# Kernel optimization log

Measured on AMD Instinct MI355X. Metric: run time of the kernel, lower is better.

## Reference

```python
import jax, jax.numpy as jnp
import numpy as np

EPS = 1e-6

def setup_inputs() -> dict:
    key = jax.random.key(0)
    kq, kk, kv = jax.random.split(key, 3)
    B, N, D = 4, 4096, 1024
    Q = jax.random.normal(kq, (B, N, D), dtype=jnp.float32)
    K = jax.random.normal(kk, (B, N, D), dtype=jnp.float32)
    V = jax.random.normal(kv, (B, N, D), dtype=jnp.float32)
    return {"Q": Q, "K": K, "V": V}

def reference(Q, K, V):
    # phi(x) = elu(x) + 1
    phi = lambda x: jax.nn.elu(x) + 1.0
    Q_phi = phi(Q)                                   # [B,N,D]
    K_phi = phi(K)                                   # [B,N,D]
    K_sum = K_phi.sum(axis=1)                        # [B,D]
    Z = jnp.einsum('bnd,bd->bn', Q_phi, K_sum) + EPS # [B,N]
    KV = jnp.einsum('bnd,bne->bde', K_phi, V)        # [B,D,E]
    context = jnp.einsum('bnd,bde->bne', Q_phi, KV)  # [B,N,E]
    out = context / Z[..., None]
    return out  # dropout is identity at inference (rate set to 0)
```

## Files before the change

kernel.cpp:

```cpp
#include <hip/hip_runtime.h>

#define BATCH 4
#define SEQ   4096
#define DIM   1024
#define EPS_F 1e-6f
#define KSPLIT 4

typedef __bf16 bf16_t;
typedef bf16_t bf16x8 __attribute__((ext_vector_type(8)));
typedef float  f32x4  __attribute__((ext_vector_type(4)));
typedef unsigned short u16x8 __attribute__((ext_vector_type(8)));

__device__ __forceinline__ unsigned short f2bf(float f) {
  unsigned u = __float_as_uint(f);
  u += 0x7FFFu + ((u >> 16) & 1u);
  return (unsigned short)(u >> 16);
}
__device__ __forceinline__ float bf2f(unsigned short h) {
  return __uint_as_float(((unsigned)h) << 16);
}
__device__ __forceinline__ float phi_f(float x) {
  return x > 0.f ? x + 1.f : __expf(x);
}

__global__ __launch_bounds__(256) void zero_f32(float* __restrict__ p, int n) {
  const int i = blockIdx.x * 256 + threadIdx.x;
  if (i < n) p[i] = 0.f;
}

template<bool PHI, bool KSUM>
__global__ __launch_bounds__(256) void phi_transpose(const float* __restrict__ in,
    unsigned short* __restrict__ out, float* __restrict__ ksum, int rows, int cols) {
  __shared__ float t[32][33];
  __shared__ float ps[8][32];
  const int bx = blockIdx.x * 32;
  const int by = blockIdx.y * 32;
  const size_t bo = (size_t)blockIdx.z * rows * cols;
  const int x = threadIdx.x, y = threadIdx.y;
  #pragma unroll
  for (int j = 0; j < 32; j += 8) {
    float v = in[bo + (size_t)(by + y + j) * cols + bx + x];
    if (PHI) v = phi_f(v);
    t[y + j][x] = v;
  }
  __syncthreads();
  #pragma unroll
  for (int j = 0; j < 32; j += 8)
    out[bo + (size_t)(bx + y + j) * rows + by + x] = f2bf(t[x][y + j]);
  if (KSUM) {
    float s = t[y][x] + t[y + 8][x] + t[y + 16][x] + t[y + 24][x];
    ps[y][x] = s;
    __syncthreads();
    if (y == 0) {
      float tot = 0.f;
      #pragma unroll
      for (int j = 0; j < 8; ++j) tot += ps[j][x];
      atomicAdd(&ksum[(size_t)blockIdx.z * cols + bx + x], tot);
    }
  }
}

__global__ __launch_bounds__(256) void phi_cast_qz(const float* __restrict__ Q,
    const float* __restrict__ Ksum, unsigned short* __restrict__ Qp,
    float* __restrict__ invZ) {
  const int row  = blockIdx.x * 4 + (threadIdx.x >> 6);
  const int lane = threadIdx.x & 63;
  const int b = row >> 12;
  const float* q  = Q + (size_t)row * DIM;
  const float* ks = Ksum + (size_t)b * DIM;
  float s = 0.f;
  #pragma unroll
  for (int c = 0; c < 2; ++c) {
    const int d0 = c * 512 + lane * 8;
    float4 v0 = *(const float4*)(q + d0);
    float4 v1 = *(const float4*)(q + d0 + 4);
    float4 k0 = *(const float4*)(ks + d0);
    float4 k1 = *(const float4*)(ks + d0 + 4);
    u16x8 o;
    o[0] = f2bf(phi_f(v0.x)); s += bf2f(o[0]) * k0.x;
    o[1] = f2bf(phi_f(v0.y)); s += bf2f(o[1]) * k0.y;
    o[2] = f2bf(phi_f(v0.z)); s += bf2f(o[2]) * k0.z;
    o[3] = f2bf(phi_f(v0.w)); s += bf2f(o[3]) * k0.w;
    o[4] = f2bf(phi_f(v1.x)); s += bf2f(o[4]) * k1.x;
    o[5] = f2bf(phi_f(v1.y)); s += bf2f(o[5]) * k1.y;
    o[6] = f2bf(phi_f(v1.z)); s += bf2f(o[6]) * k1.z;
    o[7] = f2bf(phi_f(v1.w)); s += bf2f(o[7]) * k1.w;
    *(u16x8*)(Qp + (size_t)row * DIM + d0) = o;
  }
  #pragma unroll
  for (int off = 32; off > 0; off >>= 1) s += __shfl_down(s, off);
  if (lane == 0) invZ[row] = 1.0f / (s + EPS_F);
}

__global__ __launch_bounds__(256) void reduce_kv(const unsigned short* __restrict__ P,
    unsigned short* __restrict__ KVt) {
  const size_t per = (size_t)DIM * DIM;
  const size_t i = ((size_t)blockIdx.x * 256 + threadIdx.x) * 8;
  const size_t b = blockIdx.y;
  const unsigned short* p = P + b * KSPLIT * per + i;
  float s[8] = {};
  #pragma unroll
  for (int sp = 0; sp < KSPLIT; ++sp) {
    u16x8 v = *(const u16x8*)(p + sp * per);
    #pragma unroll
    for (int j = 0; j < 8; ++j) s[j] += bf2f(v[j]);
  }
  u16x8 o;
  #pragma unroll
  for (int j = 0; j < 8; ++j) o[j] = f2bf(s[j]);
  *(u16x8*)(KVt + b * per + i) = o;
}

#define GLD(gp, lp) __builtin_amdgcn_global_load_lds( \
    (const __attribute__((address_space(1))) unsigned int*)(gp), \
    (__attribute__((address_space(3))) unsigned int*)(lp), 16, 0, 0)
#define BARRIER __builtin_amdgcn_s_barrier()
#define WAITV(n) asm volatile("s_waitcnt vmcnt(" #n ")" ::: "memory")

template<int EPI, int KS>
__global__ __launch_bounds__(512, 2) void gemm256_bt(
    const unsigned short* __restrict__ A, const unsigned short* __restrict__ Bm,
    void* __restrict__ Cv, const float* __restrict__ invZ,
    int M, int Nc, int K, int gx, int gy) {
  extern __shared__ unsigned short lds[];
  unsigned short* const As0 = lds;
  unsigned short* const As1 = lds + 16384;
  unsigned short* const Bs0 = lds + 32768;
  unsigned short* const Bs1 = lds + 49152;

  const int t    = threadIdx.x;
  const int wid  = t >> 6;
  const int lane = t & 63;
  const int id   = blockIdx.x;
  const int sw   = (id & 7) * (gridDim.x >> 3) + (id >> 3);
  const int bxi  = sw % gx;
  const int rem  = sw / gx;
  const int byi  = rem % gy;
  const int bz   = rem / gy;
  const int brow = byi * 256, bcol = bxi * 256;
  const size_t batch = bz / KS;
  const int split = bz % KS;
  const int Kc = K / KS;
  const unsigned short* Ab = A + batch * ((size_t)M * K) + (size_t)brow * K + (size_t)split * Kc;
  const unsigned short* Bb = Bm + batch * ((size_t)Nc * K) + (size_t)bcol * K + (size_t)split * Kc;

  const int srow_t = t >> 3;
  const int c_src  = (t & 7) ^ (srow_t & 7);
  const unsigned short* gA = Ab + (size_t)srow_t * K + c_src * 8;
  const unsigned short* gB = Bb + (size_t)((srow_t >> 5) * 64 + (srow_t & 31)) * K + c_src * 8;
  const int ldsAu = wid * 512;
  const int ldsBu = wid * 512 + (wid >> 2) * 2048;

  auto stageA = [&](unsigned short* D, int h, int kt) {
    GLD(gA + (size_t)(h * 64) * K + (size_t)kt * 64,       D + (h * 64) * 64 + ldsAu);
    GLD(gA + (size_t)(128 + h * 64) * K + (size_t)kt * 64, D + (128 + h * 64) * 64 + ldsAu);
  };
  auto stageB = [&](unsigned short* D, int h, int kt) {
    GLD(gB + (size_t)(h * 32) * K + (size_t)kt * 64,       D + (h * 32) * 64 + ldsBu);
    GLD(gB + (size_t)(128 + h * 32) * K + (size_t)kt * 64, D + (128 + h * 32) * 64 + ldsBu);
  };

  const int fr  = lane & 15;
  const int g   = lane >> 4;
  const int wrw = (wid >> 2) * 128;
  const int wcw = (wid & 3) * 64;
  const int ck0 = ((g)     ^ (fr & 7)) * 8;
  const int ck1 = ((4 + g) ^ (fr & 7)) * 8;

  f32x4 acc[8][4] = {};
  bf16x8 af[4][2], bf0[2][2], bf1[2][2];

#define LOADA(S, mh) { _Pragma("unroll") for (int m_ = 0; m_ < 4; ++m_) { \
    const int ro_ = (wrw + ((mh) * 4 + m_) * 16 + fr) * 64; \
    af[m_][0] = *(const bf16x8*)((S) + ro_ + ck0); \
    af[m_][1] = *(const bf16x8*)((S) + ro_ + ck1); } }
#define LOADB(S, nh, BF) { _Pragma("unroll") for (int n_ = 0; n_ < 2; ++n_) { \
    const int ro_ = (wcw + (nh) * 32 + n_ * 16 + fr) * 64; \
    BF[n_][0] = *(const bf16x8*)((S) + ro_ + ck0); \
    BF[n_][1] = *(const bf16x8*)((S) + ro_ + ck1); } }
#define QUAD(mh, nh, BF) { __builtin_amdgcn_s_setprio(1); \
    _Pragma("unroll") for (int m_ = 0; m_ < 4; ++m_) \
    _Pragma("unroll") for (int n_ = 0; n_ < 2; ++n_) \
    _Pragma("unroll") for (int k_ = 0; k_ < 2; ++k_) \
      acc[(mh) * 4 + m_][(nh) * 2 + n_] = __builtin_amdgcn_mfma_f32_16x16x32_bf16( \
          af[m_][k_], BF[n_][k_], acc[(mh) * 4 + m_][(nh) * 2 + n_], 0, 0, 0); \
    __builtin_amdgcn_s_setprio(0); }

  stageA(As0, 0, 0); stageB(Bs0, 0, 0); stageB(Bs0, 1, 0); stageA(As0, 1, 0);
  stageA(As1, 0, 1); stageB(Bs1, 0, 1); stageB(Bs1, 1, 1);
  WAITV(6);
  BARRIER;

  const int NITER = Kc >> 7;
  for (int i = 0; i < NITER - 1; ++i) {
    const int k2 = 2 * i;
    LOADA(As0, 0); LOADB(Bs0, 0, bf0); stageA(As1, 1, k2 + 1);
    BARRIER; QUAD(0, 0, bf0); BARRIER;
    LOADB(Bs0, 1, bf1); stageA(As0, 0, k2 + 2);
    BARRIER; QUAD(0, 1, bf1); BARRIER;
    LOADA(As0, 1); stageB(Bs0, 0, k2 + 2);
    BARRIER; QUAD(1, 0, bf0); BARRIER;
    stageB(Bs0, 1, k2 + 2); WAITV(6);
    BARRIER; QUAD(1, 1, bf1); BARRIER;
    LOADA(As1, 0); LOADB(Bs1, 0, bf0); stageA(As0, 1, k2 + 2);
    BARRIER; QUAD(0, 0, bf0); BARRIER;
    LOADB(Bs1, 1, bf1); stageA(As1, 0, k2 + 3);
    BARRIER; QUAD(0, 1, bf1); BARRIER;
    LOADA(As1, 1); stageB(Bs1, 0, k2 + 3);
    BARRIER; QUAD(1, 0, bf0); BARRIER;
    stageB(Bs1, 1, k2 + 3); WAITV(6);
    BARRIER; QUAD(1, 1, bf1); BARRIER;
  }
  {
    const int k2 = 2 * (NITER - 1);
    LOADA(As0, 0); LOADB(Bs0, 0, bf0); stageA(As1, 1, k2 + 1);
    BARRIER; QUAD(0, 0, bf0); BARRIER;
    LOADB(Bs0, 1, bf1);
    BARRIER; QUAD(0, 1, bf1); BARRIER;
    LOADA(As0, 1);
    BARRIER; QUAD(1, 0, bf0); BARRIER;
    WAITV(0);
    BARRIER; QUAD(1, 1, bf1); BARRIER;
    LOADA(As1, 0); LOADB(Bs1, 0, bf0);
    BARRIER; QUAD(0, 0, bf0); BARRIER;
    LOADB(Bs1, 1, bf1);
    BARRIER; QUAD(0, 1, bf1); BARRIER;
    LOADA(As1, 1);
    BARRIER; QUAD(1, 0, bf0); BARRIER;
    QUAD(1, 1, bf1);
  }
#undef LOADA
#undef LOADB
#undef QUAD

  if (EPI == 0) {
    unsigned short* Cb = (unsigned short*)Cv + (size_t)bz * M * Nc;
    #pragma unroll
    for (int m = 0; m < 8; ++m) {
      const int row = brow + wrw + m * 16 + g * 4;
      #pragma unroll
      for (int r = 0; r < 4; ++r)
        #pragma unroll
        for (int n = 0; n < 4; ++n)
          Cb[(size_t)(row + r) * Nc + bcol + wcw + n * 16 + fr] = f2bf(acc[m][n][r]);
    }
  } else {
    float* Cb = (float*)Cv + batch * ((size_t)M * Nc);
    const float* zb = invZ + batch * (size_t)M;
    #pragma unroll
    for (int m = 0; m < 8; ++m) {
      const int row = brow + wrw + m * 16 + g * 4;
      #pragma unroll
      for (int r = 0; r < 4; ++r) {
        const float z = zb[row + r];
        #pragma unroll
        for (int n = 0; n < 4; ++n)
          Cb[(size_t)(row + r) * Nc + bcol + wcw + n * 16 + fr] = acc[m][n][r] * z;
      }
    }
  }
}

extern "C" void kernel_launch(void* const* d_in, const int* in_sizes, int n_in,
                              void* d_out, int out_size, void* d_ws, size_t ws_size,
                              hipStream_t stream) {
  const float* Q = (const float*)d_in[0];
  const float* K = (const float*)d_in[1];
  const float* V = (const float*)d_in[2];
  float* out = (float*)d_out;

  char* ws = (char*)d_ws;
  size_t off = 0;
  auto alloc = [&](size_t bytes) {
    void* p = ws + off;
    off += (bytes + 255) & ~(size_t)255;
    return p;
  };
  unsigned short* Qp   = (unsigned short*)alloc((size_t)BATCH * SEQ * DIM * 2);
  unsigned short* P    = Qp;
  unsigned short* Kt   = (unsigned short*)alloc((size_t)BATCH * SEQ * DIM * 2);
  unsigned short* Vt   = (unsigned short*)alloc((size_t)BATCH * SEQ * DIM * 2);
  unsigned short* KVt  = (unsigned short*)alloc((size_t)BATCH * DIM * DIM * 2);
  float* Ksum = (float*)alloc((size_t)BATCH * DIM * 4);
  float* invZ = (float*)alloc((size_t)BATCH * SEQ * 4);

  hipFuncSetAttribute(reinterpret_cast<const void*>(&gemm256_bt<0, KSPLIT>),
                      hipFuncAttributeMaxDynamicSharedMemorySize, 131072);
  hipFuncSetAttribute(reinterpret_cast<const void*>(&gemm256_bt<1, 1>),
                      hipFuncAttributeMaxDynamicSharedMemorySize, 131072);

  const dim3 tb(32, 8);
  zero_f32<<<(BATCH * DIM + 255) / 256, 256, 0, stream>>>(Ksum, BATCH * DIM);
  phi_transpose<true, true ><<<dim3(DIM / 32, SEQ / 32, BATCH), tb, 0, stream>>>(K, Kt, Ksum, SEQ, DIM);
  phi_transpose<false, false><<<dim3(DIM / 32, SEQ / 32, BATCH), tb, 0, stream>>>(V, Vt, nullptr, SEQ, DIM);
  gemm256_bt<0, KSPLIT><<<(DIM / 256) * (DIM / 256) * BATCH * KSPLIT, 512, 131072, stream>>>(
      Vt, Kt, P, nullptr, DIM, DIM, SEQ, DIM / 256, DIM / 256);
  reduce_kv<<<dim3(DIM * DIM / (256 * 8), BATCH), 256, 0, stream>>>(P, KVt);
  phi_cast_qz<<<BATCH * SEQ / 4, 256, 0, stream>>>(Q, Ksum, Qp, invZ);
  gemm256_bt<1, 1><<<(DIM / 256) * (SEQ / 256) * BATCH, 512, 131072, stream>>>(
      Qp, KVt, out, invZ, SEQ, DIM, DIM, DIM / 256, SEQ / 256);
}
```

Before: 146.4 us.

## Rework GEMM main loop with double-buffered register fragments and pointer-swapped LDS

The GEMM main loop is rewritten to process one K-tile per iteration with ping-pong LDS buffers swapped by pointer. A and B register fragments are now double-buffered so the next fragment's LDS read is issued before the current MFMA block. The tile count becomes a compile-time template parameter with a non-unrolled loop and a peeled two-tile tail. This aims to hide LDS read latency behind MFMAs and cut code size, at the cost of more VGPRs under a 2-waves-per-SIMD launch bound and a hardcoded tile count of 16, which must equal K/64 for both GEMMs (K=4096/4 and K=1024 both give 16).

```diff
diff --git a/kernel.cpp b/kernel.cpp
--- a/kernel.cpp
+++ b/kernel.cpp
@@ -117,7 +117,7 @@
 #define BARRIER __builtin_amdgcn_s_barrier()
 #define WAITV(n) asm volatile("s_waitcnt vmcnt(" #n ")" ::: "memory")
 
-template<int EPI, int KS>
+template<int EPI, int KS, int NT>
 __global__ __launch_bounds__(512, 2) void gemm256_bt(
     const unsigned short* __restrict__ A, const unsigned short* __restrict__ Bm,
     void* __restrict__ Cv, const float* __restrict__ invZ,
@@ -168,70 +168,78 @@
   const int ck1 = ((4 + g) ^ (fr & 7)) * 8;
 
   f32x4 acc[8][4] = {};
-  bf16x8 af[4][2], bf0[2][2], bf1[2][2];
-
-#define LOADA(S, mh) { _Pragma("unroll") for (int m_ = 0; m_ < 4; ++m_) { \
+  bf16x8 afX[4][2], afY[4][2], bfX[2][2], bfY[2][2];
+
+#define LDA(S, mh, DST) { _Pragma("unroll") for (int m_ = 0; m_ < 4; ++m_) { \
     const int ro_ = (wrw + ((mh) * 4 + m_) * 16 + fr) * 64; \
-    af[m_][0] = *(const bf16x8*)((S) + ro_ + ck0); \
-    af[m_][1] = *(const bf16x8*)((S) + ro_ + ck1); } }
-#define LOADB(S, nh, BF) { _Pragma("unroll") for (int n_ = 0; n_ < 2; ++n_) { \
+    DST[m_][0] = *(const bf16x8*)((S) + ro_ + ck0); \
+    DST[m_][1] = *(const bf16x8*)((S) + ro_ + ck1); } }
+#define LDBF(S, nh, DST) { _Pragma("unroll") for (int n_ = 0; n_ < 2; ++n_) { \
     const int ro_ = (wcw + (nh) * 32 + n_ * 16 + fr) * 64; \
-    BF[n_][0] = *(const bf16x8*)((S) + ro_ + ck0); \
-    BF[n_][1] = *(const bf16x8*)((S) + ro_ + ck1); } }
-#define QUAD(mh, nh, BF) { __builtin_amdgcn_s_setprio(1); \
+    DST[n_][0] = *(const bf16x8*)((S) + ro_ + ck0); \
+    DST[n_][1] = *(const bf16x8*)((S) + ro_ + ck1); } }
+#define MM(mh, nh, AF, BF) { __builtin_amdgcn_s_setprio(1); \
     _Pragma("unroll") for (int m_ = 0; m_ < 4; ++m_) \
     _Pragma("unroll") for (int n_ = 0; n_ < 2; ++n_) \
     _Pragma("unroll") for (int k_ = 0; k_ < 2; ++k_) \
       acc[(mh) * 4 + m_][(nh) * 2 + n_] = __builtin_amdgcn_mfma_f32_16x16x32_bf16( \
-          af[m_][k_], BF[n_][k_], acc[(mh) * 4 + m_][(nh) * 2 + n_], 0, 0, 0); \
+          AF[m_][k_], BF[n_][k_], acc[(mh) * 4 + m_][(nh) * 2 + n_], 0, 0, 0); \
     __builtin_amdgcn_s_setprio(0); }
 
-  stageA(As0, 0, 0); stageB(Bs0, 0, 0); stageB(Bs0, 1, 0); stageA(As0, 1, 0);
-  stageA(As1, 0, 1); stageB(Bs1, 0, 1); stageB(Bs1, 1, 1);
-  WAITV(6);
+  unsigned short *Ac = As0, *An = As1, *Bc = Bs0, *Bn = Bs1;
+
+  stageA(Ac, 0, 0); stageB(Bc, 0, 0); stageB(Bc, 1, 0); stageA(Ac, 1, 0);
+  stageA(An, 0, 1); stageB(Bn, 0, 1); stageB(Bn, 1, 1);
+  stageA(An, 1, 1);
+  WAITV(8);
   BARRIER;
-
-  const int NITER = Kc >> 7;
-  for (int i = 0; i < NITER - 1; ++i) {
-    const int k2 = 2 * i;
-    LOADA(As0, 0); LOADB(Bs0, 0, bf0); stageA(As1, 1, k2 + 1);
-    BARRIER; QUAD(0, 0, bf0); BARRIER;
-    LOADB(Bs0, 1, bf1); stageA(As0, 0, k2 + 2);
-    BARRIER; QUAD(0, 1, bf1); BARRIER;
-    LOADA(As0, 1); stageB(Bs0, 0, k2 + 2);
-    BARRIER; QUAD(1, 0, bf0); BARRIER;
-    stageB(Bs0, 1, k2 + 2); WAITV(6);
-    BARRIER; QUAD(1, 1, bf1); BARRIER;
-    LOADA(As1, 0); LOADB(Bs1, 0, bf0); stageA(As0, 1, k2 + 2);
-    BARRIER; QUAD(0, 0, bf0); BARRIER;
-    LOADB(Bs1, 1, bf1); stageA(As1, 0, k2 + 3);
-    BARRIER; QUAD(0, 1, bf1); BARRIER;
-    LOADA(As1, 1); stageB(Bs1, 0, k2 + 3);
-    BARRIER; QUAD(1, 0, bf0); BARRIER;
-    stageB(Bs1, 1, k2 + 3); WAITV(6);
-    BARRIER; QUAD(1, 1, bf1); BARRIER;
-  }
+  LDA(Ac, 0, afX); LDBF(Bc, 0, bfX);
+
+  #pragma unroll 1
+  for (int it = 0; it < NT - 2; ++it) {
+    const int t2 = it + 2;
+    LDBF(Bc, 1, bfY);
+    stageA(Ac, 0, t2);
+    BARRIER; MM(0, 0, afX, bfX); BARRIER;
+    stageB(Bc, 0, t2);
+    WAITV(6);
+    BARRIER;
+    LDA(Ac, 1, afY);
+    MM(0, 1, afX, bfY); BARRIER;
+    LDA(An, 0, afX);
+    stageB(Bc, 1, t2);
+    BARRIER; MM(1, 0, afY, bfX); BARRIER;
+    LDBF(Bn, 0, bfX);
+    stageA(Ac, 1, t2);
+    BARRIER; MM(1, 1, afY, bfY); BARRIER;
+    unsigned short* tp;
+    tp = Ac; Ac = An; An = tp;
+    tp = Bc; Bc = Bn; Bn = tp;
+  }
+  LDBF(Bc, 1, bfY);
+  BARRIER; MM(0, 0, afX, bfX); BARRIER;
+  WAITV(0);
+  BARRIER;
+  LDA(Ac, 1, afY);
+  MM(0, 1, afX, bfY); BARRIER;
+  LDA(An, 0, afX);
+  BARRIER; MM(1, 0, afY, bfX); BARRIER;
+  LDBF(Bn, 0, bfX);
+  BARRIER; MM(1, 1, afY, bfY); BARRIER;
   {
-    const int k2 = 2 * (NITER - 1);
-    LOADA(As0, 0); LOADB(Bs0, 0, bf0); stageA(As1, 1, k2 + 1);
-    BARRIER; QUAD(0, 0, bf0); BARRIER;
-    LOADB(Bs0, 1, bf1);
-    BARRIER; QUAD(0, 1, bf1); BARRIER;
-    LOADA(As0, 1);
-    BARRIER; QUAD(1, 0, bf0); BARRIER;
-    WAITV(0);
-    BARRIER; QUAD(1, 1, bf1); BARRIER;
-    LOADA(As1, 0); LOADB(Bs1, 0, bf0);
-    BARRIER; QUAD(0, 0, bf0); BARRIER;
-    LOADB(Bs1, 1, bf1);
-    BARRIER; QUAD(0, 1, bf1); BARRIER;
-    LOADA(As1, 1);
-    BARRIER; QUAD(1, 0, bf0); BARRIER;
-    QUAD(1, 1, bf1);
-  }
-#undef LOADA
-#undef LOADB
-#undef QUAD
+    unsigned short* tp;
+    tp = Ac; Ac = An; An = tp;
+    tp = Bc; Bc = Bn; Bn = tp;
+  }
+  LDBF(Bc, 1, bfY);
+  BARRIER; MM(0, 0, afX, bfX);
+  LDA(Ac, 1, afY);
+  MM(0, 1, afX, bfY);
+  MM(1, 0, afY, bfX);
+  MM(1, 1, afY, bfY);
+#undef LDA
+#undef LDBF
+#undef MM
 
   if (EPI == 0) {
     unsigned short* Cb = (unsigned short*)Cv + (size_t)bz * M * Nc;
@@ -284,19 +292,19 @@
   float* Ksum = (float*)alloc((size_t)BATCH * DIM * 4);
   float* invZ = (float*)alloc((size_t)BATCH * SEQ * 4);
 
-  hipFuncSetAttribute(reinterpret_cast<const void*>(&gemm256_bt<0, KSPLIT>),
+  hipFuncSetAttribute(reinterpret_cast<const void*>(&gemm256_bt<0, KSPLIT, 16>),
                       hipFuncAttributeMaxDynamicSharedMemorySize, 131072);
-  hipFuncSetAttribute(reinterpret_cast<const void*>(&gemm256_bt<1, 1>),
+  hipFuncSetAttribute(reinterpret_cast<const void*>(&gemm256_bt<1, 1, 16>),
                       hipFuncAttributeMaxDynamicSharedMemorySize, 131072);
 
   const dim3 tb(32, 8);
   zero_f32<<<(BATCH * DIM + 255) / 256, 256, 0, stream>>>(Ksum, BATCH * DIM);
   phi_transpose<true, true ><<<dim3(DIM / 32, SEQ / 32, BATCH), tb, 0, stream>>>(K, Kt, Ksum, SEQ, DIM);
   phi_transpose<false, false><<<dim3(DIM / 32, SEQ / 32, BATCH), tb, 0, stream>>>(V, Vt, nullptr, SEQ, DIM);
-  gemm256_bt<0, KSPLIT><<<(DIM / 256) * (DIM / 256) * BATCH * KSPLIT, 512, 131072, stream>>>(
+  gemm256_bt<0, KSPLIT, 16><<<(DIM / 256) * (DIM / 256) * BATCH * KSPLIT, 512, 131072, stream>>>(
       Vt, Kt, P, nullptr, DIM, DIM, SEQ, DIM / 256, DIM / 256);
   reduce_kv<<<dim3(DIM * DIM / (256 * 8), BATCH), 256, 0, stream>>>(P, KVt);
   phi_cast_qz<<<BATCH * SEQ / 4, 256, 0, stream>>>(Q, Ksum, Qp, invZ);
-  gemm256_bt<1, 1><<<(DIM / 256) * (SEQ / 256) * BATCH, 512, 131072, stream>>>(
+  gemm256_bt<1, 1, 16><<<(DIM / 256) * (SEQ / 256) * BATCH, 512, 131072, stream>>>(
       Qp, KVt, out, invZ, SEQ, DIM, DIM, DIM / 256, SEQ / 256);
 }
```

Measured after the change: 146.7 us. About the same (+0.2%).

## Load B operand directly from global into registers, stage only A in LDS

Applied to the files above, without the earlier changes.

The GEMM kernel stops staging the B tile through LDS. Each wave now loads its B fragments straight from global memory into double-buffered registers, while only A is double-buffered in LDS, one barrier per k-tile. The schedule shrinks from eight barrier-separated quarter phases per two tiles to a simpler per-tile pipeline, and the dynamic LDS request drops to 64 KB static. The trade-off is more register pressure (launch bounds drop to one block per CU) and uncoalesced, redundant per-wave global reads of B, since waves sharing columns each fetch the same data.

```diff
diff --git a/kernel.cpp b/kernel.cpp
--- a/kernel.cpp
+++ b/kernel.cpp
@@ -117,16 +117,13 @@
 #define BARRIER __builtin_amdgcn_s_barrier()
 #define WAITV(n) asm volatile("s_waitcnt vmcnt(" #n ")" ::: "memory")
 
-template<int EPI, int KS>
-__global__ __launch_bounds__(512, 2) void gemm256_bt(
+template<int EPI, int KS, int NT>
+__global__ __launch_bounds__(512, 1) void gemm256g(
     const unsigned short* __restrict__ A, const unsigned short* __restrict__ Bm,
     void* __restrict__ Cv, const float* __restrict__ invZ,
     int M, int Nc, int K, int gx, int gy) {
-  extern __shared__ unsigned short lds[];
-  unsigned short* const As0 = lds;
-  unsigned short* const As1 = lds + 16384;
-  unsigned short* const Bs0 = lds + 32768;
-  unsigned short* const Bs1 = lds + 49152;
+  __shared__ unsigned short As0[16384];
+  __shared__ unsigned short As1[16384];
 
   const int t    = threadIdx.x;
   const int wid  = t >> 6;
@@ -147,17 +144,12 @@
   const int srow_t = t >> 3;
   const int c_src  = (t & 7) ^ (srow_t & 7);
   const unsigned short* gA = Ab + (size_t)srow_t * K + c_src * 8;
-  const unsigned short* gB = Bb + (size_t)((srow_t >> 5) * 64 + (srow_t & 31)) * K + c_src * 8;
   const int ldsAu = wid * 512;
-  const int ldsBu = wid * 512 + (wid >> 2) * 2048;
-
-  auto stageA = [&](unsigned short* D, int h, int kt) {
-    GLD(gA + (size_t)(h * 64) * K + (size_t)kt * 64,       D + (h * 64) * 64 + ldsAu);
-    GLD(gA + (size_t)(128 + h * 64) * K + (size_t)kt * 64, D + (128 + h * 64) * 64 + ldsAu);
-  };
-  auto stageB = [&](unsigned short* D, int h, int kt) {
-    GLD(gB + (size_t)(h * 32) * K + (size_t)kt * 64,       D + (h * 32) * 64 + ldsBu);
-    GLD(gB + (size_t)(128 + h * 32) * K + (size_t)kt * 64, D + (128 + h * 32) * 64 + ldsBu);
+
+  auto stageA = [&](unsigned short* D, int kt) {
+    #pragma unroll
+    for (int i2 = 0; i2 < 4; ++i2)
+      GLD(gA + (size_t)(i2 * 64) * K + (size_t)kt * 64, D + (i2 * 64) * 64 + ldsAu);
   };
 
   const int fr  = lane & 15;
@@ -167,71 +159,61 @@
   const int ck0 = ((g)     ^ (fr & 7)) * 8;
   const int ck1 = ((4 + g) ^ (fr & 7)) * 8;
 
+  const unsigned short* rb[2][2];
+  #pragma unroll
+  for (int nh = 0; nh < 2; ++nh)
+    #pragma unroll
+    for (int n2 = 0; n2 < 2; ++n2)
+      rb[nh][n2] = Bb + (size_t)(wcw + nh * 32 + n2 * 16 + fr) * K + g * 8;
+
   f32x4 acc[8][4] = {};
-  bf16x8 af[4][2], bf0[2][2], bf1[2][2];
-
-#define LOADA(S, mh) { _Pragma("unroll") for (int m_ = 0; m_ < 4; ++m_) { \
+  bf16x8 af[4][2], bfA[2][2][2], bfB[2][2][2];
+
+#define LOADA_(S, mh) { _Pragma("unroll") for (int m_ = 0; m_ < 4; ++m_) { \
     const int ro_ = (wrw + ((mh) * 4 + m_) * 16 + fr) * 64; \
     af[m_][0] = *(const bf16x8*)((S) + ro_ + ck0); \
     af[m_][1] = *(const bf16x8*)((S) + ro_ + ck1); } }
-#define LOADB(S, nh, BF) { _Pragma("unroll") for (int n_ = 0; n_ < 2; ++n_) { \
-    const int ro_ = (wcw + (nh) * 32 + n_ * 16 + fr) * 64; \
-    BF[n_][0] = *(const bf16x8*)((S) + ro_ + ck0); \
-    BF[n_][1] = *(const bf16x8*)((S) + ro_ + ck1); } }
-#define QUAD(mh, nh, BF) { __builtin_amdgcn_s_setprio(1); \
+#define ISSUEB_(DST, ktv) { _Pragma("unroll") for (int nh_ = 0; nh_ < 2; ++nh_) \
+    _Pragma("unroll") for (int n2_ = 0; n2_ < 2; ++n2_) \
+    _Pragma("unroll") for (int kk_ = 0; kk_ < 2; ++kk_) \
+      DST[nh_][n2_][kk_] = *(const bf16x8*)(rb[nh_][n2_] + (size_t)(ktv) * 64 + kk_ * 32); }
+#define QUADX_(mh, nh, BF) { __builtin_amdgcn_s_setprio(1); \
     _Pragma("unroll") for (int m_ = 0; m_ < 4; ++m_) \
     _Pragma("unroll") for (int n_ = 0; n_ < 2; ++n_) \
     _Pragma("unroll") for (int k_ = 0; k_ < 2; ++k_) \
       acc[(mh) * 4 + m_][(nh) * 2 + n_] = __builtin_amdgcn_mfma_f32_16x16x32_bf16( \
-          af[m_][k_], BF[n_][k_], acc[(mh) * 4 + m_][(nh) * 2 + n_], 0, 0, 0); \
+          af[m_][k_], BF[nh][n_][k_], acc[(mh) * 4 + m_][(nh) * 2 + n_], 0, 0, 0); \
     __builtin_amdgcn_s_setprio(0); }
-
-  stageA(As0, 0, 0); stageB(Bs0, 0, 0); stageB(Bs0, 1, 0); stageA(As0, 1, 0);
-  stageA(As1, 0, 1); stageB(Bs1, 0, 1); stageB(Bs1, 1, 1);
-  WAITV(6);
-  BARRIER;
-
-  const int NITER = Kc >> 7;
-  for (int i = 0; i < NITER - 1; ++i) {
-    const int k2 = 2 * i;
-    LOADA(As0, 0); LOADB(Bs0, 0, bf0); stageA(As1, 1, k2 + 1);
-    BARRIER; QUAD(0, 0, bf0); BARRIER;
-    LOADB(Bs0, 1, bf1); stageA(As0, 0, k2 + 2);
-    BARRIER; QUAD(0, 1, bf1); BARRIER;
-    LOADA(As0, 1); stageB(Bs0, 0, k2 + 2);
-    BARRIER; QUAD(1, 0, bf0); BARRIER;
-    stageB(Bs0, 1, k2 + 2); WAITV(6);
-    BARRIER; QUAD(1, 1, bf1); BARRIER;
-    LOADA(As1, 0); LOADB(Bs1, 0, bf0); stageA(As0, 1, k2 + 2);
-    BARRIER; QUAD(0, 0, bf0); BARRIER;
-    LOADB(Bs1, 1, bf1); stageA(As1, 0, k2 + 3);
-    BARRIER; QUAD(0, 1, bf1); BARRIER;
-    LOADA(As1, 1); stageB(Bs1, 0, k2 + 3);
-    BARRIER; QUAD(1, 0, bf0); BARRIER;
-    stageB(Bs1, 1, k2 + 3); WAITV(6);
-    BARRIER; QUAD(1, 1, bf1); BARRIER;
-  }
-  {
-    const int k2 = 2 * (NITER - 1);
-    LOADA(As0, 0); LOADB(Bs0, 0, bf0); stageA(As1, 1, k2 + 1);
-    BARRIER; QUAD(0, 0, bf0); BARRIER;
-    LOADB(Bs0, 1, bf1);
-    BARRIER; QUAD(0, 1, bf1); BARRIER;
-    LOADA(As0, 1);
-    BARRIER; QUAD(1, 0, bf0); BARRIER;
-    WAITV(0);
-    BARRIER; QUAD(1, 1, bf1); BARRIER;
-    LOADA(As1, 0); LOADB(Bs1, 0, bf0);
-    BARRIER; QUAD(0, 0, bf0); BARRIER;
-    LOADB(Bs1, 1, bf1);
-    BARRIER; QUAD(0, 1, bf1); BARRIER;
-    LOADA(As1, 1);
-    BARRIER; QUAD(1, 0, bf0); BARRIER;
-    QUAD(1, 1, bf1);
-  }
-#undef LOADA
-#undef LOADB
-#undef QUAD
+#define TILE_FULL(CUR, NXT, SP, SN) { \
+    WAITV(8); BARRIER; \
+    LOADA_(SP, 0); \
+    stageA(SN, kt + 1); \
+    ISSUEB_(NXT, kt + 1); \
+    WAITV(12); \
+    QUADX_(0, 0, CUR); QUADX_(0, 1, CUR); \
+    LOADA_(SP, 1); \
+    QUADX_(1, 0, CUR); QUADX_(1, 1, CUR); \
+    ++kt; }
+
+  int kt = 0;
+  stageA(As0, 0);
+  ISSUEB_(bfA, 0);
+  #pragma unroll 1
+  for (int i = 0; i < NT / 2 - 1; ++i) {
+    TILE_FULL(bfA, bfB, As0, As1);
+    TILE_FULL(bfB, bfA, As1, As0);
+  }
+  TILE_FULL(bfA, bfB, As0, As1);
+  WAITV(8); BARRIER;
+  LOADA_(As1, 0);
+  WAITV(0);
+  QUADX_(0, 0, bfB); QUADX_(0, 1, bfB);
+  LOADA_(As1, 1);
+  QUADX_(1, 0, bfB); QUADX_(1, 1, bfB);
+#undef LOADA_
+#undef ISSUEB_
+#undef QUADX_
+#undef TILE_FULL
 
   if (EPI == 0) {
     unsigned short* Cb = (unsigned short*)Cv + (size_t)bz * M * Nc;
@@ -284,19 +266,14 @@
   float* Ksum = (float*)alloc((size_t)BATCH * DIM * 4);
   float* invZ = (float*)alloc((size_t)BATCH * SEQ * 4);
 
-  hipFuncSetAttribute(reinterpret_cast<const void*>(&gemm256_bt<0, KSPLIT>),
-                      hipFuncAttributeMaxDynamicSharedMemorySize, 131072);
-  hipFuncSetAttribute(reinterpret_cast<const void*>(&gemm256_bt<1, 1>),
-                      hipFuncAttributeMaxDynamicSharedMemorySize, 131072);
-
   const dim3 tb(32, 8);
   zero_f32<<<(BATCH * DIM + 255) / 256, 256, 0, stream>>>(Ksum, BATCH * DIM);
   phi_transpose<true, true ><<<dim3(DIM / 32, SEQ / 32, BATCH), tb, 0, stream>>>(K, Kt, Ksum, SEQ, DIM);
   phi_transpose<false, false><<<dim3(DIM / 32, SEQ / 32, BATCH), tb, 0, stream>>>(V, Vt, nullptr, SEQ, DIM);
-  gemm256_bt<0, KSPLIT><<<(DIM / 256) * (DIM / 256) * BATCH * KSPLIT, 512, 131072, stream>>>(
+  gemm256g<0, KSPLIT, 16><<<(DIM / 256) * (DIM / 256) * BATCH * KSPLIT, 512, 0, stream>>>(
       Vt, Kt, P, nullptr, DIM, DIM, SEQ, DIM / 256, DIM / 256);
   reduce_kv<<<dim3(DIM * DIM / (256 * 8), BATCH), 256, 0, stream>>>(P, KVt);
   phi_cast_qz<<<BATCH * SEQ / 4, 256, 0, stream>>>(Q, Ksum, Qp, invZ);
-  gemm256_bt<1, 1><<<(DIM / 256) * (SEQ / 256) * BATCH, 512, 131072, stream>>>(
+  gemm256g<1, 1, 16><<<(DIM / 256) * (SEQ / 256) * BATCH, 512, 0, stream>>>(
       Qp, KVt, out, invZ, SEQ, DIM, DIM, DIM / 256, SEQ / 256);
 }
```

Result: slower. 194.1 us (+32.5%).
